# Optimization experiments

Hardware: AMD Instinct MI355X
Metric: run time of the kernel (lower is better)

Reference implementation:

```python
import jax, jax.numpy as jnp
from jax import lax
import numpy as np

B, H, W, DIM = 16, 56, 56, 128
DI, K, R, N = 128, 4, 4, 1  # d_inner, directions, dt_rank, d_state


def setup_inputs() -> dict:
    key = jax.random.key(0)
    ks = jax.random.split(key, 8)
    x = jax.random.normal(ks[0], (B, H, W, DIM), dtype=jnp.float32)
    in_proj_w = jax.random.normal(ks[1], (2 * DI, DIM), dtype=jnp.float32) * 0.02
    conv_w = jax.random.normal(ks[2], (DI, 1, 3, 3), dtype=jnp.float32) * 0.1  # depthwise 3x3
    conv_b = jnp.zeros((DI,), dtype=jnp.float32)
    x_proj_w = jax.random.normal(ks[3], (K, R + 2 * N, DI), dtype=jnp.float32) * 0.02
    dt_proj_w = jax.random.normal(ks[4], (K, DI, R), dtype=jnp.float32) * 0.1
    dt_proj_b = jax.random.normal(ks[5], (K, DI), dtype=jnp.float32) * 0.1
    A_log = jnp.log(jax.random.uniform(ks[6], (K, DI, N), minval=0.5, maxval=4.0))
    Ds = jnp.ones((K, DI), dtype=jnp.float32)
    out_norm_w = jnp.ones((DI,), dtype=jnp.float32)
    out_norm_b = jnp.zeros((DI,), dtype=jnp.float32)
    return {"x": x, "in_proj_w": in_proj_w, "conv_w": conv_w, "conv_b": conv_b,
            "x_proj_w": x_proj_w, "dt_proj_w": dt_proj_w, "dt_proj_b": dt_proj_b,
            "A_log": A_log, "Ds": Ds, "out_norm_w": out_norm_w, "out_norm_b": out_norm_b}


def _ss2d(x, in_proj_w, conv_w, conv_b, x_proj_w, dt_proj_w, dt_proj_b, A_log, Ds, out_norm_w, out_norm_b):
    b, h, w, _ = x.shape
    L = h * w
    # in_proj (no bias) -> split into ssm branch and gate z
    xz = x @ in_proj_w.T                      # (B,H,W,2*DI)
    xi, z = jnp.split(xz, 2, axis=-1)
    # depthwise conv 3x3 + SiLU
    xc = jnp.transpose(xi, (0, 3, 1, 2))      # (B,DI,H,W)
    xc = lax.conv_general_dilated(xc, conv_w, (1, 1), 'SAME',
                                  feature_group_count=DI,
                                  dimension_numbers=('NCHW', 'OIHW', 'NCHW'))
    xc = jax.nn.silu(xc + conv_b[None, :, None, None])
    # 4-directional cross-scan: h, h_flip, v (transpose), v_flip
    x_hw = xc.reshape(b, DI, L)
    x_wh = jnp.transpose(xc, (0, 1, 3, 2)).reshape(b, DI, L)
    xs = jnp.stack([x_hw, jnp.flip(x_hw, -1), x_wh, jnp.flip(x_wh, -1)], axis=1)  # (B,K,DI,L)
    # per-direction input-dependent dt, B, C
    x_dbl = jnp.einsum('bkdl,kcd->bkcl', xs, x_proj_w)            # (B,K,R+2N,L)
    dt_r, Bm, Cm = jnp.split(x_dbl, [R, R + N], axis=2)
    dt = jnp.einsum('bkrl,kdr->bkdl', dt_r, dt_proj_w) + dt_proj_b[None, :, :, None]
    dt = jax.nn.softplus(dt)                                      # (B,K,DI,L)
    A = -jnp.exp(A_log)                                           # (K,DI,N)
    dA = jnp.exp(dt[..., None] * A[None, :, :, None, :])          # (B,K,DI,L,N)
    dBu = dt[..., None] * jnp.swapaxes(Bm, 2, 3)[:, :, None, :, :] * xs[..., None]
    # sequential selective scan over L (vectorized over B,K,DI,N)
    dA_l = jnp.moveaxis(dA, 3, 0)                                 # (L,B,K,DI,N)
    dBu_l = jnp.moveaxis(dBu, 3, 0)
    C_l = jnp.moveaxis(Cm, 3, 0)                                  # (L,B,K,N)

    def step(hst, inp):
        da, dbu, c = inp
        hst = da * hst + dbu
        y = jnp.sum(hst * c[:, :, None, :], axis=-1)              # (B,K,DI)
        return hst, y

    h0 = jnp.zeros((b, K, DI, N), dtype=x.dtype)
    _, ys = lax.scan(step, h0, (dA_l, dBu_l, C_l))                # ys: (L,B,K,DI)
    y = jnp.transpose(ys, (1, 2, 3, 0)) + Ds[None, :, :, None] * xs  # (B,K,DI,L)
    # merge directions back to row-major and sum
    y_h = y[:, 0]
    y_hf = jnp.flip(y[:, 1], -1)
    y_v = jnp.transpose(y[:, 2].reshape(b, DI, w, h), (0, 1, 3, 2)).reshape(b, DI, L)
    y_vf = jnp.transpose(jnp.flip(y[:, 3], -1).reshape(b, DI, w, h), (0, 1, 3, 2)).reshape(b, DI, L)
    ysum = (y_h + y_hf + y_v + y_vf).reshape(b, DI, h, w)
    ysum = jnp.transpose(ysum, (0, 2, 3, 1))                      # (B,H,W,DI)
    # out LayerNorm + gate
    mu = jnp.mean(ysum, axis=-1, keepdims=True)
    var = jnp.mean(jnp.square(ysum - mu), axis=-1, keepdims=True)
    yn = (ysum - mu) * lax.rsqrt(var + 1e-5) * out_norm_w + out_norm_b
    return yn * jax.nn.silu(z)                                    # (B,H,W,DI)


def reference(x, in_proj_w, conv_w, conv_b, x_proj_w, dt_proj_w, dt_proj_b, A_log, Ds, out_norm_w, out_norm_b):
    y = _ss2d(x, in_proj_w, conv_w, conv_b, x_proj_w, dt_proj_w, dt_proj_b, A_log, Ds, out_norm_w, out_norm_b)
    # adaptive avg pool to (1,1) then flatten -> (B, DI)
    return jnp.mean(y, axis=(1, 2))
```

## Files before the change

### kernel.cpp

```cpp
#include <hip/hip_runtime.h>
#include <math.h>

#define BB   16
#define HHH  56
#define WWW  56
#define LL   3136
#define DI_  128
#define KK   4
#define NCH  196
#define CS   16

#define OFF_XI   ((size_t)0)
#define OFF_ZS   ((size_t)6422528)
#define OFF_XC   ((size_t)12845056)
#define OFF_XDN  ((size_t)19267584)
#define OFF_PA   ((size_t)20873216)
#define OFF_HL   ((size_t)22478848)
#define OFF_H0   ((size_t)24084480)
#define OFF_CWT  ((size_t)25690112)

typedef short s16x8 __attribute__((ext_vector_type(8)));
typedef float f32x4 __attribute__((ext_vector_type(4)));

__device__ __forceinline__ float sigmoidf_(float x) { return 1.0f / (1.0f + __expf(-x)); }
__device__ __forceinline__ float softplus_(float x) {
    return fmaxf(x, 0.0f) + __logf(1.0f + __expf(-fabsf(x)));
}

__device__ __forceinline__ void bf16split(float f, short* hi, short* lo) {
    unsigned u = __float_as_uint(f);
    unsigned r = u + 0x7FFFu + ((u >> 16) & 1u);
    *hi = (short)(r >> 16);
    float hf = __uint_as_float(r & 0xFFFF0000u);
    float l  = f - hf;
    unsigned u2 = __float_as_uint(l);
    unsigned r2 = u2 + 0x7FFFu + ((u2 >> 16) & 1u);
    *lo = (short)(r2 >> 16);
}

__global__ __launch_bounds__(256) void k_wsplit(const float* __restrict__ Wp,
                                                const float* __restrict__ cw,
                                                short* __restrict__ Whi,
                                                short* __restrict__ Wlo,
                                                float* __restrict__ cwT)
{
    const int idx = blockIdx.x * 256 + threadIdx.x;
    if (idx < 256 * 128) {
        short h, l;
        bf16split(Wp[idx], &h, &l);
        Whi[idx] = h;
        Wlo[idx] = l;
    }
    if (idx < 9 * 128) {
        const int t = idx >> 7;
        const int d = idx & 127;
        cwT[t * 128 + d] = cw[d * 9 + t];
    }
}

#define APAD 136
__global__ __launch_bounds__(256) void k_inproj(const float* __restrict__ x,
                                                const short* __restrict__ Whi,
                                                const short* __restrict__ Wlo,
                                                float* __restrict__ xi,
                                                float* __restrict__ zs)
{
    __shared__ short Ahi[32 * APAD];
    __shared__ short Alo[32 * APAD];
    const int tid  = threadIdx.x;
    const int row0 = blockIdx.x * 32;

#pragma unroll
    for (int i = 0; i < 4; ++i) {
        const int idx4 = i * 256 + tid;
        const int row  = idx4 >> 5;
        const int k4   = (idx4 & 31) * 4;
        float4 v = *(const float4*)&x[(size_t)(row0 + row) * 128 + k4];
        const float f[4] = {v.x, v.y, v.z, v.w};
#pragma unroll
        for (int j = 0; j < 4; ++j) {
            short h, l;
            bf16split(f[j], &h, &l);
            Ahi[row * APAD + k4 + j] = h;
            Alo[row * APAD + k4 + j] = l;
        }
    }
    __syncthreads();

    const int w    = tid >> 6;
    const int lane = tid & 63;
    const int lr   = lane & 15;
    const int lk   = (lane >> 4) * 8;

    for (int cg = 0; cg < 4; ++cg) {
        const int col0 = cg * 64 + w * 16;
        s16x8 bhi[4], blo[4];
#pragma unroll
        for (int ks = 0; ks < 4; ++ks) {
            const size_t wo = (size_t)(col0 + lr) * 128 + ks * 32 + lk;
            bhi[ks] = *(const s16x8*)&Whi[wo];
            blo[ks] = *(const s16x8*)&Wlo[wo];
        }
#pragma unroll
        for (int rt = 0; rt < 2; ++rt) {
            f32x4 acc = {0.f, 0.f, 0.f, 0.f};
#pragma unroll
            for (int ks = 0; ks < 4; ++ks) {
                const int ao = (rt * 16 + lr) * APAD + ks * 32 + lk;
                s16x8 ahi = *(const s16x8*)&Ahi[ao];
                s16x8 alo = *(const s16x8*)&Alo[ao];
                acc = __builtin_amdgcn_mfma_f32_16x16x32_bf16(alo, bhi[ks], acc, 0, 0, 0);
                acc = __builtin_amdgcn_mfma_f32_16x16x32_bf16(ahi, blo[ks], acc, 0, 0, 0);
                acc = __builtin_amdgcn_mfma_f32_16x16x32_bf16(ahi, bhi[ks], acc, 0, 0, 0);
            }
            const int col = col0 + lr;
#pragma unroll
            for (int j = 0; j < 4; ++j) {
                const size_t row = row0 + rt * 16 + (lane >> 4) * 4 + j;
                const float v = acc[j];
                if (col < 128) {
                    xi[row * 128 + col] = v;
                } else {
                    zs[row * 128 + (col - 128)] = v * sigmoidf_(v);
                }
            }
        }
    }
}

__global__ __launch_bounds__(256) void k_conv4(const float* __restrict__ xi,
                                               const float* __restrict__ cwT,
                                               const float* __restrict__ cb,
                                               float* __restrict__ xc)
{
    const int wid = (blockIdx.x & 7) * 196 + (blockIdx.x >> 3);
    const int idx = wid * 256 + threadIdx.x;
    const int d0  = (idx & 31) * 4;
    int rest = idx >> 5;
    const int w  = rest % WWW;
    rest /= WWW;
    const int hq = rest % 14;
    const int b  = rest / 14;
    const int h0 = hq * 4;

    float4 wt[9];
#pragma unroll
    for (int t = 0; t < 9; ++t) wt[t] = *(const float4*)&cwT[t * 128 + d0];
    const float4 bias = *(const float4*)&cb[d0];

    float4 a0 = bias, a1 = bias, a2 = bias, a3 = bias;
    const float* base = &xi[(size_t)b * LL * 128 + d0];
#pragma unroll
    for (int dr = -1; dr <= 4; ++dr) {
        const int hh = h0 + dr;
        if (hh < 0 || hh >= HHH) continue;
#pragma unroll
        for (int dc = -1; dc <= 1; ++dc) {
            const int ww = w + dc;
            if (ww < 0 || ww >= WWW) continue;
            const float4 v = *(const float4*)&base[(size_t)(hh * WWW + ww) * 128];
#pragma unroll
            for (int r = 0; r < 4; ++r) {
                const int tap = dr - r;
                if (tap < -1 || tap > 1) continue;
                const float4 wv = wt[(tap + 1) * 3 + (dc + 1)];
                float4* a = (r == 0) ? &a0 : (r == 1) ? &a1 : (r == 2) ? &a2 : &a3;
                a->x = fmaf(v.x, wv.x, a->x);
                a->y = fmaf(v.y, wv.y, a->y);
                a->z = fmaf(v.z, wv.z, a->z);
                a->w = fmaf(v.w, wv.w, a->w);
            }
        }
    }
    float4 av[4] = {a0, a1, a2, a3};
#pragma unroll
    for (int r = 0; r < 4; ++r) {
        float4 o;
        o.x = av[r].x * sigmoidf_(av[r].x);
        o.y = av[r].y * sigmoidf_(av[r].y);
        o.z = av[r].z * sigmoidf_(av[r].z);
        o.w = av[r].w * sigmoidf_(av[r].w);
        *(float4*)&xc[((size_t)b * LL + (h0 + r) * WWW + w) * 128 + d0] = o;
    }
}

__global__ __launch_bounds__(256) void k_projN(const float* __restrict__ xc,
                                               const float* __restrict__ xpw,
                                               float* __restrict__ xdn)
{
    __shared__ float xs[64 * 129];
    __shared__ float wl[24 * 128];
    const int tid = threadIdx.x;
    const int b   = blockIdx.x / 49;
    const int p0  = (blockIdx.x % 49) * 64;

    for (int i = tid; i < 24 * 128; i += 256) wl[i] = xpw[i];

#pragma unroll
    for (int i = 0; i < 8; ++i) {
        const int idx4 = i * 256 + tid;
        const int row  = idx4 >> 5;
        const int d4   = (idx4 & 31) * 4;
        float4 v = *(const float4*)&xc[((size_t)b * LL + p0 + row) * 128 + d4];
        xs[row * 129 + d4 + 0] = v.x;
        xs[row * 129 + d4 + 1] = v.y;
        xs[row * 129 + d4 + 2] = v.z;
        xs[row * 129 + d4 + 3] = v.w;
    }
    __syncthreads();

    const int ks   = tid >> 6;
    const int lane = tid & 63;
    float a0 = 0.f, a1 = 0.f, a2 = 0.f, a3 = 0.f, a4 = 0.f, a5 = 0.f;
    const float* wb = &wl[ks * 6 * 128];
#pragma unroll 4
    for (int d = 0; d < 128; ++d) {
        const float xv = xs[lane * 129 + d];
        a0 = fmaf(xv, wb[0 * 128 + d], a0);
        a1 = fmaf(xv, wb[1 * 128 + d], a1);
        a2 = fmaf(xv, wb[2 * 128 + d], a2);
        a3 = fmaf(xv, wb[3 * 128 + d], a3);
        a4 = fmaf(xv, wb[4 * 128 + d], a4);
        a5 = fmaf(xv, wb[5 * 128 + d], a5);
    }
    float* o = &xdn[((size_t)(b * LL + p0 + lane)) * 32 + ks * 8];
    o[0] = a0; o[1] = a1; o[2] = a2; o[3] = a3; o[4] = a4; o[5] = a5;
}

__global__ __launch_bounds__(128) void k_scan1m(const float* __restrict__ xc,
                                                const float* __restrict__ xdn,
                                                const float* __restrict__ dtw_g,
                                                const float* __restrict__ dtb_g,
                                                const float* __restrict__ alog,
                                                float* __restrict__ Pa,
                                                float* __restrict__ Hl)
{
    __shared__ float xds[CS * 16];
    const int mode = blockIdx.x / (BB * NCH);
    const int rem  = blockIdx.x % (BB * NCH);
    const int b = rem / NCH;
    const int c = rem % NCH;
    const int d = threadIdx.x;
    const int c2 = NCH - 1 - c;
    const int l0a = c * CS;
    const int kA = mode * 2;
    const int kB = kA + 1;
    const int bkA = b * 4 + kA, bkB = b * 4 + kB;

    const float* xcb  = &xc[(size_t)b * LL * 128];
    const float* base = &xdn[(size_t)b * LL * 32];

    if (d < CS * 4) {
        const int row = d >> 2;
        const int q   = (d & 3) * 4;
        int prow;
        if (mode == 0) prow = l0a + row;
        else { const int l = l0a + row; prow = (l % HHH) * WWW + (l / HHH); }
        *(float4*)&xds[row * 16 + q] = *(const float4*)&base[(size_t)prow * 32 + mode * 16 + q];
    }
    __syncthreads();

    int pj[CS];
    if (mode == 0) {
#pragma unroll
        for (int i = 0; i < CS; ++i) pj[i] = l0a + i;
    } else {
#pragma unroll
        for (int i = 0; i < CS; ++i) {
            const int l = l0a + i;
            pj[i] = (l % HHH) * WWW + (l / HHH);
        }
    }
    float xv[CS];
#pragma unroll
    for (int i = 0; i < CS; ++i) xv[i] = xcb[(size_t)pj[i] * 128 + d];

    const float A0 = dtw_g[(kA * 128 + d) * 4 + 0];
    const float A1 = dtw_g[(kA * 128 + d) * 4 + 1];
    const float A2 = dtw_g[(kA * 128 + d) * 4 + 2];
    const float A3 = dtw_g[(kA * 128 + d) * 4 + 3];
    const float Ab = dtb_g[kA * 128 + d];
    const float An = -__expf(alog[kA * 128 + d]);
    const float B0 = dtw_g[(kB * 128 + d) * 4 + 0];
    const float B1 = dtw_g[(kB * 128 + d) * 4 + 1];
    const float B2 = dtw_g[(kB * 128 + d) * 4 + 2];
    const float B3 = dtw_g[(kB * 128 + d) * 4 + 3];
    const float Bb = dtb_g[kB * 128 + d];
    const float Bn = -__expf(alog[kB * 128 + d]);

    float PA = 1.0f, hA = 0.0f, PB = 1.0f, hB = 0.0f;
#pragma unroll
    for (int i = 0; i < CS; ++i) {
        const int j = CS - 1 - i;
        const float* rA = &xds[i * 16];
        const float* rB = &xds[j * 16 + 8];
        const float drawA = fmaf(rA[0], A0, fmaf(rA[1], A1, fmaf(rA[2], A2, fmaf(rA[3], A3, Ab))));
        const float drawB = fmaf(rB[0], B0, fmaf(rB[1], B1, fmaf(rB[2], B2, fmaf(rB[3], B3, Bb))));
        const float dtA = softplus_(drawA);
        const float dtB = softplus_(drawB);
        const float dAA = __expf(dtA * An);
        const float dAB = __expf(dtB * Bn);
        PA *= dAA;
        PB *= dAB;
        hA = fmaf(dAA, hA, dtA * rA[4] * xv[i]);
        hB = fmaf(dAB, hB, dtB * rB[4] * xv[j]);
    }
    Pa[((size_t)bkA * NCH + c)  * 128 + d] = PA;
    Hl[((size_t)bkA * NCH + c)  * 128 + d] = hA;
    Pa[((size_t)bkB * NCH + c2) * 128 + d] = PB;
    Hl[((size_t)bkB * NCH + c2) * 128 + d] = hB;
}

__global__ __launch_bounds__(128) void k_scan2(const float* __restrict__ Pa,
                                               const float* __restrict__ Hl,
                                               float* __restrict__ H0)
{
    const int bk = blockIdx.x;
    const int d  = threadIdx.x;
    float h = 0.0f;
#pragma unroll 14
    for (int c = 0; c < NCH; ++c) {
        const size_t o = ((size_t)bk * NCH + c) * 128 + d;
        H0[o] = h;
        h = fmaf(Pa[o], h, Hl[o]);
    }
}

__global__ __launch_bounds__(128) void k_scan3a(const float* __restrict__ xc,
                                                const float* __restrict__ xdn,
                                                const float* __restrict__ dtw_g,
                                                const float* __restrict__ dtb_g,
                                                const float* __restrict__ alog,
                                                const float* __restrict__ ds_g,
                                                const float* __restrict__ H0,
                                                float* __restrict__ ysum)
{
    __shared__ float xds[CS * 16];
    const int b = blockIdx.x / NCH;
    const int c = blockIdx.x % NCH;
    const int d = threadIdx.x;
    const int c2 = NCH - 1 - c;
    const int bk0 = b * 4 + 0, bk1 = b * 4 + 1;
    const int l0a = c * CS;

    const float* xcb  = &xc[(size_t)b * LL * 128];
    const float* base = &xdn[(size_t)b * LL * 32];
    float* yb = &ysum[(size_t)b * LL * 128];

    if (d < CS * 4) {
        const int row = d >> 2;
        const int q   = (d & 3) * 4;
        *(float4*)&xds[row * 16 + q] = *(const float4*)&base[(size_t)(l0a + row) * 32 + q];
    }
    __syncthreads();

    float xv[CS];
#pragma unroll
    for (int i = 0; i < CS; ++i) xv[i] = xcb[(size_t)(l0a + i) * 128 + d];

    const float A0 = dtw_g[(0 * 128 + d) * 4 + 0];
    const float A1 = dtw_g[(0 * 128 + d) * 4 + 1];
    const float A2 = dtw_g[(0 * 128 + d) * 4 + 2];
    const float A3 = dtw_g[(0 * 128 + d) * 4 + 3];
    const float Ab = dtb_g[0 * 128 + d];
    const float An = -__expf(alog[0 * 128 + d]);
    const float AD = ds_g[0 * 128 + d];
    const float B0 = dtw_g[(1 * 128 + d) * 4 + 0];
    const float B1 = dtw_g[(1 * 128 + d) * 4 + 1];
    const float B2 = dtw_g[(1 * 128 + d) * 4 + 2];
    const float B3 = dtw_g[(1 * 128 + d) * 4 + 3];
    const float Bb = dtb_g[1 * 128 + d];
    const float Bn = -__expf(alog[1 * 128 + d]);
    const float BD = ds_g[1 * 128 + d];

    float y[CS];
#pragma unroll
    for (int i = 0; i < CS; ++i) y[i] = 0.0f;

    float hA = H0[((size_t)bk0 * NCH + c)  * 128 + d];
    float hB = H0[((size_t)bk1 * NCH + c2) * 128 + d];
#pragma unroll
    for (int i = 0; i < CS; ++i) {
        const int j = CS - 1 - i;
        const float* rA = &xds[i * 16];
        const float* rB = &xds[j * 16 + 8];
        const float drawA = fmaf(rA[0], A0, fmaf(rA[1], A1, fmaf(rA[2], A2, fmaf(rA[3], A3, Ab))));
        const float drawB = fmaf(rB[0], B0, fmaf(rB[1], B1, fmaf(rB[2], B2, fmaf(rB[3], B3, Bb))));
        const float dtA = softplus_(drawA);
        const float dtB = softplus_(drawB);
        const float dAA = __expf(dtA * An);
        const float dAB = __expf(dtB * Bn);
        hA = fmaf(dAA, hA, dtA * rA[4] * xv[i]);
        hB = fmaf(dAB, hB, dtB * rB[4] * xv[j]);
        y[i] += fmaf(hA, rA[5], AD * xv[i]);
        y[j] += fmaf(hB, rB[5], BD * xv[j]);
    }
#pragma unroll
    for (int i = 0; i < CS; ++i)
        yb[(size_t)(l0a + i) * 128 + d] = y[i];
}

#define YPAD 129
__global__ __launch_bounds__(128) void k_scan3bf(const float* __restrict__ xc,
                                                 const float* __restrict__ xdn,
                                                 const float* __restrict__ dtw_g,
                                                 const float* __restrict__ dtb_g,
                                                 const float* __restrict__ alog,
                                                 const float* __restrict__ ds_g,
                                                 const float* __restrict__ H0,
                                                 const float* __restrict__ ysum,
                                                 const float* __restrict__ zs,
                                                 const float* __restrict__ onw,
                                                 const float* __restrict__ onb,
                                                 float* __restrict__ out)
{
    __shared__ float xds[CS * 16];
    __shared__ float yl[CS * YPAD];
    __shared__ float muS[CS];
    __shared__ float rsS[CS];
    const int b = blockIdx.x / NCH;
    const int c = blockIdx.x % NCH;
    const int d = threadIdx.x;
    const int c2 = NCH - 1 - c;
    const int bk2 = b * 4 + 2, bk3 = b * 4 + 3;
    const int l0a = c * CS;

    const float* xcb  = &xc[(size_t)b * LL * 128];
    const float* base = &xdn[(size_t)b * LL * 32];
    const float* yb   = &ysum[(size_t)b * LL * 128];
    const float* zb   = &zs[(size_t)b * LL * 128];

    if (d < CS * 4) {
        const int row = d >> 2;
        const int q   = (d & 3) * 4;
        const int l   = l0a + row;
        const int prow = (l % HHH) * WWW + (l / HHH);
        *(float4*)&xds[row * 16 + q] = *(const float4*)&base[(size_t)prow * 32 + 16 + q];
    }
    __syncthreads();

    int pj[CS];
#pragma unroll
    for (int i = 0; i < CS; ++i) {
        const int l = l0a + i;
        pj[i] = (l % HHH) * WWW + (l / HHH);
    }
    float xv[CS];
#pragma unroll
    for (int i = 0; i < CS; ++i) xv[i] = xcb[(size_t)pj[i] * 128 + d];

    const float A0 = dtw_g[(2 * 128 + d) * 4 + 0];
    const float A1 = dtw_g[(2 * 128 + d) * 4 + 1];
    const float A2 = dtw_g[(2 * 128 + d) * 4 + 2];
    const float A3 = dtw_g[(2 * 128 + d) * 4 + 3];
    const float Ab = dtb_g[2 * 128 + d];
    const float An = -__expf(alog[2 * 128 + d]);
    const float AD = ds_g[2 * 128 + d];
    const float B0 = dtw_g[(3 * 128 + d) * 4 + 0];
    const float B1 = dtw_g[(3 * 128 + d) * 4 + 1];
    const float B2 = dtw_g[(3 * 128 + d) * 4 + 2];
    const float B3 = dtw_g[(3 * 128 + d) * 4 + 3];
    const float Bb = dtb_g[3 * 128 + d];
    const float Bn = -__expf(alog[3 * 128 + d]);
    const float BD = ds_g[3 * 128 + d];

    float y[CS];
#pragma unroll
    for (int i = 0; i < CS; ++i) y[i] = 0.0f;

    float hA = H0[((size_t)bk2 * NCH + c)  * 128 + d];
    float hB = H0[((size_t)bk3 * NCH + c2) * 128 + d];
#pragma unroll
    for (int i = 0; i < CS; ++i) {
        const int j = CS - 1 - i;
        const float* rA = &xds[i * 16];
        const float* rB = &xds[j * 16 + 8];
        const float drawA = fmaf(rA[0], A0, fmaf(rA[1], A1, fmaf(rA[2], A2, fmaf(rA[3], A3, Ab))));
        const float drawB = fmaf(rB[0], B0, fmaf(rB[1], B1, fmaf(rB[2], B2, fmaf(rB[3], B3, Bb))));
        const float dtA = softplus_(drawA);
        const float dtB = softplus_(drawB);
        const float dAA = __expf(dtA * An);
        const float dAB = __expf(dtB * Bn);
        hA = fmaf(dAA, hA, dtA * rA[4] * xv[i]);
        hB = fmaf(dAB, hB, dtB * rB[4] * xv[j]);
        y[i] += fmaf(hA, rA[5], AD * xv[i]);
        y[j] += fmaf(hB, rB[5], BD * xv[j]);
    }

#pragma unroll
    for (int i = 0; i < CS; ++i) {
        y[i] += yb[(size_t)pj[i] * 128 + d];
        yl[i * YPAD + d] = y[i];
    }
    __syncthreads();

    {
        const int pos = d >> 3;
        const int q   = d & 7;
        const float* yrow = &yl[pos * YPAD + q * 16];
        float sm = 0.0f;
#pragma unroll
        for (int j = 0; j < 16; ++j) sm += yrow[j];
        sm += __shfl_xor(sm, 1, 64);
        sm += __shfl_xor(sm, 2, 64);
        sm += __shfl_xor(sm, 4, 64);
        const float mu = sm * (1.0f / 128.0f);
        float sq = 0.0f;
#pragma unroll
        for (int j = 0; j < 16; ++j) { const float t = yrow[j] - mu; sq = fmaf(t, t, sq); }
        sq += __shfl_xor(sq, 1, 64);
        sq += __shfl_xor(sq, 2, 64);
        sq += __shfl_xor(sq, 4, 64);
        if (q == 0) {
            muS[pos] = mu;
            rsS[pos] = rsqrtf(sq * (1.0f / 128.0f) + 1e-5f);
        }
    }
    __syncthreads();

    const float wd = onw[d];
    const float bd = onb[d];
    float acc = 0.0f;
#pragma unroll
    for (int i = 0; i < CS; ++i) {
        const float yn = fmaf((y[i] - muS[i]) * rsS[i], wd, bd);
        acc = fmaf(yn, zb[(size_t)pj[i] * 128 + d], acc);
    }
    atomicAdd(&out[b * 128 + d], acc * (1.0f / (float)LL));
}

extern "C" void kernel_launch(void* const* d_in, const int* in_sizes, int n_in,
                              void* d_out, int out_size, void* d_ws, size_t ws_size,
                              hipStream_t stream)
{
    const float* x     = (const float*)d_in[0];
    const float* ipw   = (const float*)d_in[1];
    const float* cw    = (const float*)d_in[2];
    const float* cb    = (const float*)d_in[3];
    const float* xpw   = (const float*)d_in[4];
    const float* dtw   = (const float*)d_in[5];
    const float* dtb   = (const float*)d_in[6];
    const float* alog  = (const float*)d_in[7];
    const float* dsg   = (const float*)d_in[8];
    const float* onw   = (const float*)d_in[9];
    const float* onb   = (const float*)d_in[10];
    float* out = (float*)d_out;

    float* ws   = (float*)d_ws;
    float* xi   = ws + OFF_XI;
    float* zs   = ws + OFF_ZS;
    float* xc   = ws + OFF_XC;
    float* xdn  = ws + OFF_XDN;
    float* Pa   = ws + OFF_PA;
    float* Hl   = ws + OFF_HL;
    float* H0   = ws + OFF_H0;
    float* cwT  = ws + OFF_CWT;
    float* ysum = xi;
    short* Whi = (short*)(ws + OFF_XC);
    short* Wlo = (short*)(ws + OFF_XC + 16384);

    hipMemsetAsync(out, 0, (size_t)out_size * 4, stream);

    k_wsplit<<<128, 256, 0, stream>>>(ipw, cw, Whi, Wlo, cwT);
    k_inproj<<<1568, 256, 0, stream>>>(x, Whi, Wlo, xi, zs);

    k_conv4<<<1568, 256, 0, stream>>>(xi, cwT, cb, xc);

    k_projN<<<BB * 49, 256, 0, stream>>>(xc, xpw, xdn);

    k_scan1m<<<2 * BB * NCH, 128, 0, stream>>>(xc, xdn, dtw, dtb, alog, Pa, Hl);
    k_scan2<<<BB * KK, 128, 0, stream>>>(Pa, Hl, H0);
    k_scan3a<<<BB * NCH, 128, 0, stream>>>(xc, xdn, dtw, dtb, alog, dsg, H0, ysum);
    k_scan3bf<<<BB * NCH, 128, 0, stream>>>(xc, xdn, dtw, dtb, alog, dsg, H0, ysum,
                                            zs, onw, onb, out);
}
```

Baseline: 228.6 us.

## Pre-split x into bf16 hi/lo buffers and use one 16x16 tile per wave

Adds a separate kernel that splits the fp32 input into bf16 hi/lo arrays in global memory. The in-projection GEMM then loads its A fragments straight from those buffers instead of staging through shared memory, and each wave computes a single 16x16 output tile across a much larger grid. This removes the LDS staging and __syncthreads, but adds a full extra round trip of x through global memory. It also drops reuse of A across column tiles, so each A row is reloaded by 16 waves.

```diff
diff --git a/kernel.cpp b/kernel.cpp
--- a/kernel.cpp
+++ b/kernel.cpp
@@ -18,8 +18,11 @@
 #define OFF_HL   ((size_t)22478848)
 #define OFF_H0   ((size_t)24084480)
 #define OFF_CWT  ((size_t)25690112)
+#define OFF_XHI  ((size_t)25691264)
+#define OFF_XLO  ((size_t)28902528)
 
 typedef short s16x8 __attribute__((ext_vector_type(8)));
+typedef short s16x4 __attribute__((ext_vector_type(4)));
 typedef float f32x4 __attribute__((ext_vector_type(4)));
 
 __device__ __forceinline__ float sigmoidf_(float x) { return 1.0f / (1.0f + __expf(-x)); }
@@ -58,72 +61,73 @@
     }
 }
 
-#define APAD 136
-__global__ __launch_bounds__(256) void k_inproj(const float* __restrict__ x,
+__global__ __launch_bounds__(256) void k_splitx(const float* __restrict__ x,
+                                                short* __restrict__ xhi,
+                                                short* __restrict__ xlo)
+{
+    const size_t i4 = (size_t)blockIdx.x * 256 + threadIdx.x;
+    float4 v = *(const float4*)&x[i4 * 4];
+    const float f[4] = {v.x, v.y, v.z, v.w};
+    s16x4 h4, l4;
+#pragma unroll
+    for (int j = 0; j < 4; ++j) {
+        short h, l;
+        bf16split(f[j], &h, &l);
+        h4[j] = h;
+        l4[j] = l;
+    }
+    *(s16x4*)&xhi[i4 * 4] = h4;
+    *(s16x4*)&xlo[i4 * 4] = l4;
+}
+
+__global__ __launch_bounds__(256) void k_inproj(const short* __restrict__ xhi,
+                                                const short* __restrict__ xlo,
                                                 const short* __restrict__ Whi,
                                                 const short* __restrict__ Wlo,
                                                 float* __restrict__ xi,
                                                 float* __restrict__ zs)
 {
-    __shared__ short Ahi[32 * APAD];
-    __shared__ short Alo[32 * APAD];
-    const int tid  = threadIdx.x;
-    const int row0 = blockIdx.x * 32;
-
-#pragma unroll
-    for (int i = 0; i < 4; ++i) {
-        const int idx4 = i * 256 + tid;
-        const int row  = idx4 >> 5;
-        const int k4   = (idx4 & 31) * 4;
-        float4 v = *(const float4*)&x[(size_t)(row0 + row) * 128 + k4];
-        const float f[4] = {v.x, v.y, v.z, v.w};
-#pragma unroll
-        for (int j = 0; j < 4; ++j) {
-            short h, l;
-            bf16split(f[j], &h, &l);
-            Ahi[row * APAD + k4 + j] = h;
-            Alo[row * APAD + k4 + j] = l;
-        }
-    }
-    __syncthreads();
-
-    const int w    = tid >> 6;
-    const int lane = tid & 63;
+    const int id   = blockIdx.x * 4 + (threadIdx.x >> 6);
+    const int lane = threadIdx.x & 63;
+    const int ct   = id & 15;
+    const int rt   = id >> 4;
     const int lr   = lane & 15;
     const int lk   = (lane >> 4) * 8;
 
-    for (int cg = 0; cg < 4; ++cg) {
-        const int col0 = cg * 64 + w * 16;
-        s16x8 bhi[4], blo[4];
-#pragma unroll
-        for (int ks = 0; ks < 4; ++ks) {
-            const size_t wo = (size_t)(col0 + lr) * 128 + ks * 32 + lk;
-            bhi[ks] = *(const s16x8*)&Whi[wo];
-            blo[ks] = *(const s16x8*)&Wlo[wo];
+    const size_t arow = (size_t)(rt * 16 + lr) * 128;
+    const size_t brow = (size_t)(ct * 16 + lr) * 128;
+
+    s16x8 ahi[4], alo[4], bhi[4], blo[4];
+#pragma unroll
+    for (int ks = 0; ks < 4; ++ks) {
+        const int ko = ks * 32 + lk;
+        ahi[ks] = *(const s16x8*)&xhi[arow + ko];
+        alo[ks] = *(const s16x8*)&xlo[arow + ko];
+        bhi[ks] = *(const s16x8*)&Whi[brow + ko];
+        blo[ks] = *(const s16x8*)&Wlo[brow + ko];
+    }
+
+    f32x4 acc = {0.f, 0.f, 0.f, 0.f};
+#pragma unroll
+    for (int ks = 0; ks < 4; ++ks) {
+        acc = __builtin_amdgcn_mfma_f32_16x16x32_bf16(alo[ks], bhi[ks], acc, 0, 0, 0);
+        acc = __builtin_amdgcn_mfma_f32_16x16x32_bf16(ahi[ks], blo[ks], acc, 0, 0, 0);
+        acc = __builtin_amdgcn_mfma_f32_16x16x32_bf16(ahi[ks], bhi[ks], acc, 0, 0, 0);
+    }
+
+    const int col = ct * 16 + lr;
+    if (ct < 8) {
+#pragma unroll
+        for (int j = 0; j < 4; ++j) {
+            const size_t row = (size_t)rt * 16 + (lane >> 4) * 4 + j;
+            xi[row * 128 + col] = acc[j];
         }
-#pragma unroll
-        for (int rt = 0; rt < 2; ++rt) {
-            f32x4 acc = {0.f, 0.f, 0.f, 0.f};
-#pragma unroll
-            for (int ks = 0; ks < 4; ++ks) {
-                const int ao = (rt * 16 + lr) * APAD + ks * 32 + lk;
-                s16x8 ahi = *(const s16x8*)&Ahi[ao];
-                s16x8 alo = *(const s16x8*)&Alo[ao];
-                acc = __builtin_amdgcn_mfma_f32_16x16x32_bf16(alo, bhi[ks], acc, 0, 0, 0);
-                acc = __builtin_amdgcn_mfma_f32_16x16x32_bf16(ahi, blo[ks], acc, 0, 0, 0);
-                acc = __builtin_amdgcn_mfma_f32_16x16x32_bf16(ahi, bhi[ks], acc, 0, 0, 0);
-            }
-            const int col = col0 + lr;
-#pragma unroll
-            for (int j = 0; j < 4; ++j) {
-                const size_t row = row0 + rt * 16 + (lane >> 4) * 4 + j;
-                const float v = acc[j];
-                if (col < 128) {
-                    xi[row * 128 + col] = v;
-                } else {
-                    zs[row * 128 + (col - 128)] = v * sigmoidf_(v);
-                }
-            }
+    } else {
+#pragma unroll
+        for (int j = 0; j < 4; ++j) {
+            const size_t row = (size_t)rt * 16 + (lane >> 4) * 4 + j;
+            const float v = acc[j];
+            zs[row * 128 + (col - 128)] = v * sigmoidf_(v);
         }
     }
 }
@@ -558,11 +562,14 @@
     float* ysum = xi;
     short* Whi = (short*)(ws + OFF_XC);
     short* Wlo = (short*)(ws + OFF_XC + 16384);
+    short* xhi = (short*)(ws + OFF_XHI);
+    short* xlo = (short*)(ws + OFF_XLO);
 
     hipMemsetAsync(out, 0, (size_t)out_size * 4, stream);
 
     k_wsplit<<<128, 256, 0, stream>>>(ipw, cw, Whi, Wlo, cwT);
-    k_inproj<<<1568, 256, 0, stream>>>(x, Whi, Wlo, xi, zs);
+    k_splitx<<<6272, 256, 0, stream>>>(x, xhi, xlo);
+    k_inproj<<<12544, 256, 0, stream>>>(xhi, xlo, Whi, Wlo, xi, zs);
 
     k_conv4<<<1568, 256, 0, stream>>>(xi, cwT, cb, xc);
 
```

Measured after the change: 293.3 us. 1.28x slower.
